# Performance work log

Measured on AMD Instinct MI355X. Metric: run time of the kernel, lower is better.

Reference implementation:

```python
import jax, jax.numpy as jnp
import numpy as np

B, SQ, SK, D, DV = 8, 2048, 4096, 512, 256

def setup_inputs() -> dict:
    key = jax.random.key(0)
    k1, k2, k3, k4, k5 = jax.random.split(key, 5)
    X = jax.random.normal(k1, (B, SQ, D), dtype=jnp.float32)
    Y = jax.random.normal(k2, (SK, D), dtype=jnp.float32)
    Z = jax.random.normal(k3, (SK, D), dtype=jnp.float32)
    # Linear weights (torch stores [out, in]); scaled like default init
    W_k = jax.random.normal(k4, (D, D), dtype=jnp.float32) / np.sqrt(D)
    W_v = jax.random.normal(k5, (DV, D), dtype=jnp.float32) / np.sqrt(D)
    return {"X": X, "Y": Y, "Z": Z, "W_k": W_k, "W_v": W_v, "rate": 0}


def reference(X, Y, Z, W_k, W_v, rate):
    # key = W_k(Y).unsqueeze(0): [1, SK, D]; value = W_v(Z).unsqueeze(0): [1, SK, DV]
    key = (Y @ W_k.T)[None]
    value = (Z @ W_v.T)[None]
    # scores = X @ key^T / sqrt(d): [B, SQ, SK] (key batch dim broadcasts)
    scale = 1.0 / jnp.sqrt(jnp.asarray(X.shape[-1], dtype=X.dtype))
    scores = jnp.matmul(X, jnp.swapaxes(key, 1, 2)) * scale
    attn = jax.nn.softmax(scores, axis=-1)
    # dropout layers act as identity in eval mode
    out = jnp.matmul(attn, value)  # [B, SQ, DV]
    return out
```

## Files before the change

kernel.cpp:

```cpp
#include <hip/hip_runtime.h>
#include <hip/hip_bf16.h>

#define NB    8
#define SQN   2048
#define SKN   4096
#define DDIM  512
#define DVDIM 256
#define NROWS (NB*SQN)
#define NS    2
#define NJ    ((SKN/64)/NS)

typedef __attribute__((ext_vector_type(8)))  short bf16x8;
typedef __attribute__((ext_vector_type(4)))  short bf16x4;
typedef __attribute__((ext_vector_type(4)))  float f32x4;
typedef __attribute__((ext_vector_type(16))) float f32x16;

__device__ __forceinline__ short f2bf(float f) {
    unsigned u = __float_as_uint(f);
    return (short)((u + 0x7FFFu + ((u >> 16) & 1u)) >> 16);
}

__device__ __forceinline__ void gload_lds16(const void* g, void* l) {
    __builtin_amdgcn_global_load_lds(
        (const __attribute__((address_space(1))) unsigned int*)g,
        (__attribute__((address_space(3))) unsigned int*)l, 16, 0, 0);
}

#define BAR_VM(N_) do {                                                       \
    asm volatile("s_waitcnt vmcnt(" #N_ ")" ::: "memory");                    \
    __builtin_amdgcn_sched_barrier(0);                                        \
    __builtin_amdgcn_s_barrier();                                             \
    __builtin_amdgcn_sched_barrier(0);                                        \
} while (0)

#define BAR_LGKM() do {                                                       \
    asm volatile("s_waitcnt lgkmcnt(0)" ::: "memory");                        \
    __builtin_amdgcn_sched_barrier(0);                                        \
    __builtin_amdgcn_s_barrier();                                             \
    __builtin_amdgcn_sched_barrier(0);                                        \
} while (0)

__global__ __launch_bounds__(256, 2) void proj_gemms(
    const float* __restrict__ Y, const float* __restrict__ Z,
    const float* __restrict__ Wk, const float* __restrict__ Wv,
    unsigned short* __restrict__ keyb, unsigned short* __restrict__ vtb)
{
    __shared__ short sA[64*128];
    __shared__ short sB[64*128];
    const float *A, *Bm;
    unsigned short* C;
    int N, m0, n0;
    if (blockIdx.z == 0) {
        A = Y; Bm = Wk; C = keyb; N = DDIM;
        m0 = blockIdx.x * 64; n0 = blockIdx.y * 64;
    } else {
        int lin = blockIdx.x * 8 + blockIdx.y;
        if (lin >= 256) return;
        A = Wv; Bm = Z; C = vtb; N = SKN;
        m0 = (lin >> 6) * 64; n0 = (lin & 63) * 64;
    }
    const int tid  = threadIdx.x;
    const int wave = tid >> 6;
    const int lane = tid & 63;
    const int quad = lane >> 4;
    const int l15  = lane & 15;

    f32x4 acc[4];
    #pragma unroll
    for (int n = 0; n < 4; ++n) { acc[n][0]=0.f; acc[n][1]=0.f; acc[n][2]=0.f; acc[n][3]=0.f; }

    float4 ra[8], rb[8];
    #pragma unroll
    for (int it = 0; it < 8; ++it) {
        int f = it*1024 + tid*4, row = f >> 7, col = f & 127;
        ra[it] = *(const float4*)(A  + (size_t)(m0+row)*DDIM + col);
        rb[it] = *(const float4*)(Bm + (size_t)(n0+row)*DDIM + col);
    }

    for (int kc = 0; kc < DDIM; kc += 128) {
        __syncthreads();
        #pragma unroll
        for (int it = 0; it < 8; ++it) {
            int f = it*1024 + tid*4;
            bf16x4 a4; a4[0]=f2bf(ra[it].x); a4[1]=f2bf(ra[it].y); a4[2]=f2bf(ra[it].z); a4[3]=f2bf(ra[it].w);
            *(bf16x4*)(sA + f) = a4;
            bf16x4 b4; b4[0]=f2bf(rb[it].x); b4[1]=f2bf(rb[it].y); b4[2]=f2bf(rb[it].z); b4[3]=f2bf(rb[it].w);
            *(bf16x4*)(sB + f) = b4;
        }
        __syncthreads();
        if (kc + 128 < DDIM) {
            #pragma unroll
            for (int it = 0; it < 8; ++it) {
                int f = it*1024 + tid*4, row = f >> 7, col = f & 127;
                ra[it] = *(const float4*)(A  + (size_t)(m0+row)*DDIM + kc + 128 + col);
                rb[it] = *(const float4*)(Bm + (size_t)(n0+row)*DDIM + kc + 128 + col);
            }
        }
        #pragma unroll
        for (int t = 0; t < 4; ++t) {
            bf16x8 af = *(const bf16x8*)(sA + (wave*16 + l15)*128 + t*32 + quad*8);
            #pragma unroll
            for (int n = 0; n < 4; ++n) {
                bf16x8 bfr = *(const bf16x8*)(sB + (n*16 + l15)*128 + t*32 + quad*8);
                acc[n] = __builtin_amdgcn_mfma_f32_16x16x32_bf16(af, bfr, acc[n], 0, 0, 0);
            }
        }
    }
    #pragma unroll
    for (int n = 0; n < 4; ++n)
        #pragma unroll
        for (int r = 0; r < 4; ++r) {
            int m  = m0 + wave*16 + quad*4 + r;
            int nn = n0 + n*16 + l15;
            C[(size_t)m*N + nn] = (unsigned short)f2bf(acc[n][r]);
        }
}

__global__ __launch_bounds__(512, 2) void attn_fused(
    const float* __restrict__ X,
    const unsigned short* __restrict__ Kb,
    const unsigned short* __restrict__ Vt,
    float* __restrict__ Opart,
    float* __restrict__ Mpart,
    float* __restrict__ Lpart)
{
    __shared__ __align__(16) char smem[100352];
    char* sV   = smem + 49152;
    char* sPex = smem + 81920;
    float* sSt = (float*)(smem + 98304);

    const int tid  = threadIdx.x;
    const int wave = tid >> 6;
    const int lane = tid & 63;
    const int l31  = lane & 31;
    const int hi   = lane >> 5;
    const int wm   = wave >> 1;
    const int wk   = wave & 1;

    const int bid   = blockIdx.x;
    const int xcd   = bid & 7;
    const int slot  = bid >> 3;
    const int split = xcd >> 2;
    const int q0    = ((xcd & 3)*32 + slot) * 128;
    const float scale = 0.04419417382415922f;

    bf16x8 qf[32];
    {
        const float* xrow = X + (size_t)(q0 + wm*32 + l31)*DDIM + hi*8;
        #pragma unroll
        for (int t = 0; t < 32; ++t) {
            float4 a = *(const float4*)(xrow + t*16);
            float4 b = *(const float4*)(xrow + t*16 + 4);
            bf16x8 q;
            q[0]=f2bf(a.x*scale); q[1]=f2bf(a.y*scale); q[2]=f2bf(a.z*scale); q[3]=f2bf(a.w*scale);
            q[4]=f2bf(b.x*scale); q[5]=f2bf(b.y*scale); q[6]=f2bf(b.z*scale); q[7]=f2bf(b.w*scale);
            qf[t] = q;
        }
    }

    f32x16 o[4];
    #pragma unroll
    for (int n = 0; n < 4; ++n)
        #pragma unroll
        for (int r = 0; r < 16; ++r) o[n][r] = 0.f;
    float m_r = -1e30f, l_r = 0.f;

    const int jt0 = split * (NJ*64);

    #define STAGE_K(jtb_, cc_, bufp_)                                         \
        do {                                                                  \
            _Pragma("unroll")                                                 \
            for (int it_ = 0; it_ < 2; ++it_) {                               \
                const char* src_ = (const char*)Kb                            \
                    + (size_t)((jtb_) + it_*32 + l31)*1024                    \
                    + (cc_)*256 + wave*32 + hi*16;                            \
                gload_lds16(src_, (bufp_) + (wave*2 + it_)*1024);             \
            }                                                                 \
        } while (0)

    #define STAGE_V(jtb_)                                                     \
        do {                                                                  \
            _Pragma("unroll")                                                 \
            for (int it_ = 0; it_ < 4; ++it_) {                               \
                const char* src_ = (const char*)Vt                            \
                    + (size_t)(wave*32 + l31)*8192                            \
                    + (size_t)((jtb_) + it_*16 + hi*8)*2;                     \
                gload_lds16(src_, sV + (wave*4 + it_)*1024);                  \
            }                                                                 \
        } while (0)

    char* q0p = smem;
    char* q1p = smem + 16384;
    char* q2p = smem + 32768;

    STAGE_K(jt0, 0, q0p);
    STAGE_K(jt0, 1, q1p);

    for (int j = 0; j < NJ; ++j) {
        const int jtb = jt0 + j*64;
        f32x16 s;
        #pragma unroll
        for (int r = 0; r < 16; ++r) s[r] = 0.f;

        #pragma unroll
        for (int c = 0; c < 4; ++c) {
            if (c == 0)      BAR_VM(2);
            else if (c == 1) BAR_VM(6);
            else if (c == 2) BAR_VM(6);
            else { if (j + 1 < NJ) BAR_VM(2); else BAR_VM(0); }

            if (c == 0)      { STAGE_K(jtb, 2, q2p); STAGE_V(jtb); }
            else if (c == 1) STAGE_K(jtb, 3, q0p);
            else if (c == 2) { if (j + 1 < NJ) STAGE_K(jtb + 64, 0, q1p); }
            else             { if (j + 1 < NJ) STAGE_K(jtb + 64, 1, q2p); }

            const char* rbuf = (c == 0) ? q0p : (c == 1) ? q1p
                             : (c == 2) ? q2p : q0p;
            const char* kb = rbuf + wk*1024 + lane*16;
            __builtin_amdgcn_s_setprio(1);
            #pragma unroll
            for (int t = 0; t < 8; ++t) {
                bf16x8 kf = *(const bf16x8*)(kb + t*2048);
                s = __builtin_amdgcn_mfma_f32_32x32x16_bf16(kf, qf[c*8+t], s, 0, 0, 0);
            }
            __builtin_amdgcn_s_setprio(0);
        }

        float tmax = fmaxf(fmaxf(fmaxf(s[0],s[1]),fmaxf(s[2],s[3])),
                           fmaxf(fmaxf(s[4],s[5]),fmaxf(s[6],s[7])));
        tmax = fmaxf(tmax, fmaxf(fmaxf(fmaxf(s[8],s[9]),fmaxf(s[10],s[11])),
                                 fmaxf(fmaxf(s[12],s[13]),fmaxf(s[14],s[15]))));
        tmax = fmaxf(tmax, __shfl_xor(tmax, 32));
        if (lane < 32) sSt[(wave*2 + 0)*32 + lane] = tmax;
        BAR_LGKM();
        float tmax_o = sSt[((wave^1)*2 + 0)*32 + l31];
        const float mn = fmaxf(m_r, fmaxf(tmax, tmax_o));
        const float alpha = __expf(m_r - mn);
        float tsum = 0.f;
        #pragma unroll
        for (int r = 0; r < 16; ++r) { float pv = __expf(s[r] - mn); s[r] = pv; tsum += pv; }
        tsum += __shfl_xor(tsum, 32);

        bf16x8 pf[2];
        #pragma unroll
        for (int ks = 0; ks < 2; ++ks) {
            int wA, wB, wC, wD;
            asm("v_cvt_pk_bf16_f32 %0, %1, %2" : "=v"(wA) : "v"(s[8*ks+0]), "v"(s[8*ks+1]));
            asm("v_cvt_pk_bf16_f32 %0, %1, %2" : "=v"(wB) : "v"(s[8*ks+2]), "v"(s[8*ks+3]));
            asm("v_cvt_pk_bf16_f32 %0, %1, %2" : "=v"(wC) : "v"(s[8*ks+4]), "v"(s[8*ks+5]));
            asm("v_cvt_pk_bf16_f32 %0, %1, %2" : "=v"(wD) : "v"(s[8*ks+6]), "v"(s[8*ks+7]));
            asm("v_permlane32_swap_b32 %0, %1" : "+v"(wA), "+v"(wC));
            asm("v_permlane32_swap_b32 %0, %1" : "+v"(wB), "+v"(wD));
            union { int w[4]; bf16x8 v; } u;
            u.w[0] = wA; u.w[1] = wB; u.w[2] = wC; u.w[3] = wD;
            pf[ks] = u.v;
        }
        *(bf16x8*)(sPex + (wm*4 + wk*2 + 0)*1024 + lane*16) = pf[0];
        *(bf16x8*)(sPex + (wm*4 + wk*2 + 1)*1024 + lane*16) = pf[1];
        if (lane < 32) sSt[(wave*2 + 1)*32 + lane] = tsum;
        BAR_LGKM();
        float tsum_o = sSt[((wave^1)*2 + 1)*32 + l31];
        l_r = l_r*alpha + (tsum + tsum_o);
        m_r = mn;
        if (__any(alpha < 1.f)) {
            #pragma unroll
            for (int r = 0; r < 16; ++r) {
                int row = (r&3) + 8*(r>>2) + 4*hi;
                float ar = __shfl(alpha, row);
                #pragma unroll
                for (int n = 0; n < 4; ++n) o[n][r] *= ar;
            }
        }

        const char* vb = sV + wk*16384 + lane*16;
        const char* pb = sPex + wm*4096 + lane*16;
        __builtin_amdgcn_s_setprio(1);
        #pragma unroll
        for (int g = 0; g < 4; ++g) {
            bf16x8 pa = ((g >> 1) == wk) ? pf[g & 1]
                        : *(const bf16x8*)(pb + g*1024);
            #pragma unroll
            for (int n = 0; n < 4; ++n) {
                bf16x8 vf = *(const bf16x8*)(vb + (n*4 + g)*1024);
                o[n] = __builtin_amdgcn_mfma_f32_32x32x16_bf16(pa, vf, o[n], 0, 0, 0);
            }
        }
        __builtin_amdgcn_s_setprio(0);

        char* tp = q0p; q0p = q1p; q1p = q2p; q2p = tp;
    }
    #undef STAGE_K
    #undef STAGE_V

    const size_t base = (size_t)split * NROWS;
    const int gr0 = q0 + wm*32;
    if (wk == 0 && lane < 32) {
        Mpart[base + gr0 + lane] = m_r;
        Lpart[base + gr0 + lane] = l_r;
    }
    #pragma unroll
    for (int r = 0; r < 16; ++r) {
        int row = (r&3) + 8*(r>>2) + 4*hi;
        float* orow = Opart + (base + gr0 + row) * (size_t)DVDIM + wk*128;
        #pragma unroll
        for (int n = 0; n < 4; ++n)
            orow[n*32 + l31] = o[n][r];
    }
}

__global__ void combine_splits(
    const float* __restrict__ Opart, const float* __restrict__ Mpart,
    const float* __restrict__ Lpart, float* __restrict__ out)
{
    const int row = blockIdx.x * 4 + (threadIdx.x >> 6);
    const int dv4 = (threadIdx.x & 63) * 4;
    float M = -1e30f;
    #pragma unroll
    for (int s = 0; s < NS; ++s) M = fmaxf(M, Mpart[(size_t)s*NROWS + row]);
    float denom = 0.f;
    float4 acc = make_float4(0.f, 0.f, 0.f, 0.f);
    #pragma unroll
    for (int s = 0; s < NS; ++s) {
        float w = __expf(Mpart[(size_t)s*NROWS + row] - M);
        denom += Lpart[(size_t)s*NROWS + row] * w;
        float4 ov = *(const float4*)(Opart + ((size_t)s*NROWS + row)*DVDIM + dv4);
        acc.x += ov.x*w; acc.y += ov.y*w; acc.z += ov.z*w; acc.w += ov.w*w;
    }
    float inv = 1.0f / denom;
    *(float4*)(out + (size_t)row*DVDIM + dv4)
        = make_float4(acc.x*inv, acc.y*inv, acc.z*inv, acc.w*inv);
}

extern "C" void kernel_launch(void* const* d_in, const int* in_sizes, int n_in,
                              void* d_out, int out_size, void* d_ws, size_t ws_size,
                              hipStream_t stream) {
    const float* X  = (const float*)d_in[0];
    const float* Y  = (const float*)d_in[1];
    const float* Z  = (const float*)d_in[2];
    const float* Wk = (const float*)d_in[3];
    const float* Wv = (const float*)d_in[4];
    float* out = (float*)d_out;

    char* ws = (char*)d_ws;
    unsigned short* keyb = (unsigned short*)ws;
    unsigned short* vtb  = (unsigned short*)(ws + (4u<<20));
    float* Opart = (float*)(ws + (6u<<20));
    float* Mpart = (float*)(ws + (6u<<20) + (size_t)NS*NROWS*DVDIM*4);
    float* Lpart = Mpart + (size_t)NS*NROWS;

    proj_gemms<<<dim3(64, 8, 2), dim3(256), 0, stream>>>(Y, Z, Wk, Wv, keyb, vtb);
    attn_fused<<<dim3(256), dim3(512), 0, stream>>>(
        X, keyb, vtb, Opart, Mpart, Lpart);
    combine_splits<<<dim3(NROWS/4), dim3(256), 0, stream>>>(Opart, Mpart, Lpart, out);
}
```

Measured before the change: 266.8 us.

## Halve attention block to 64 query rows with double-buffered K staging

Shrinks each attention workgroup from 8 waves/128 query rows to 4 waves/64 rows and doubles the grid, so each wave stages twice as many K/V chunks. The K pipeline goes from a three-buffer rotation with partial waits to two alternating buffers with mostly full vmcnt waits, reducing LDS per block. The aim is more blocks per CU and finer scheduling, at the cost of loading each K/V tile twice as often overall and having less load/compute overlap.

```diff
diff --git a/kernel.cpp b/kernel.cpp
--- a/kernel.cpp
+++ b/kernel.cpp
@@ -116,7 +116,7 @@
         }
 }
 
-__global__ __launch_bounds__(512, 2) void attn_fused(
+__global__ __launch_bounds__(256, 2) void attn_fused(
     const float* __restrict__ X,
     const unsigned short* __restrict__ Kb,
     const unsigned short* __restrict__ Vt,
@@ -124,10 +124,12 @@
     float* __restrict__ Mpart,
     float* __restrict__ Lpart)
 {
-    __shared__ __align__(16) char smem[100352];
-    char* sV   = smem + 49152;
-    char* sPex = smem + 81920;
-    float* sSt = (float*)(smem + 98304);
+    __shared__ __align__(16) char smem[74752];
+    char* b0   = smem;
+    char* b1   = smem + 16384;
+    char* sV   = smem + 32768;
+    char* sPex = smem + 65536;
+    float* sSt = (float*)(smem + 73728);
 
     const int tid  = threadIdx.x;
     const int wave = tid >> 6;
@@ -141,7 +143,7 @@
     const int xcd   = bid & 7;
     const int slot  = bid >> 3;
     const int split = xcd >> 2;
-    const int q0    = ((xcd & 3)*32 + slot) * 128;
+    const int q0    = ((xcd & 3)*64 + slot) * 64;
     const float scale = 0.04419417382415922f;
 
     bf16x8 qf[32];
@@ -170,31 +172,39 @@
     #define STAGE_K(jtb_, cc_, bufp_)                                         \
         do {                                                                  \
             _Pragma("unroll")                                                 \
-            for (int it_ = 0; it_ < 2; ++it_) {                               \
+            for (int it_ = 0; it_ < 4; ++it_) {                               \
                 const char* src_ = (const char*)Kb                            \
-                    + (size_t)((jtb_) + it_*32 + l31)*1024                    \
-                    + (cc_)*256 + wave*32 + hi*16;                            \
-                gload_lds16(src_, (bufp_) + (wave*2 + it_)*1024);             \
+                    + (size_t)((jtb_) + (it_&1)*32 + l31)*1024                \
+                    + (cc_)*256 + wave*64 + (it_>>1)*32 + hi*16;              \
+                gload_lds16(src_, (bufp_) + (wave*4 + it_)*1024);             \
             }                                                                 \
         } while (0)
 
     #define STAGE_V(jtb_)                                                     \
         do {                                                                  \
             _Pragma("unroll")                                                 \
-            for (int it_ = 0; it_ < 4; ++it_) {                               \
+            for (int it_ = 0; it_ < 8; ++it_) {                               \
                 const char* src_ = (const char*)Vt                            \
-                    + (size_t)(wave*32 + l31)*8192                            \
-                    + (size_t)((jtb_) + it_*16 + hi*8)*2;                     \
-                gload_lds16(src_, sV + (wave*4 + it_)*1024);                  \
+                    + (size_t)((wave*2 + (it_>>2))*32 + l31)*8192             \
+                    + (size_t)((jtb_) + (it_&3)*16 + hi*8)*2;                 \
+                gload_lds16(src_, sV + (wave*8 + it_)*1024);                  \
             }                                                                 \
         } while (0)
 
-    char* q0p = smem;
-    char* q1p = smem + 16384;
-    char* q2p = smem + 32768;
-
-    STAGE_K(jt0, 0, q0p);
-    STAGE_K(jt0, 1, q1p);
+    #define QK8(cc_, bufp_)                                                   \
+        do {                                                                  \
+            const char* kb_ = (bufp_) + wk*1024 + lane*16;                    \
+            __builtin_amdgcn_s_setprio(1);                                    \
+            _Pragma("unroll")                                                 \
+            for (int t_ = 0; t_ < 8; ++t_) {                                  \
+                bf16x8 kf_ = *(const bf16x8*)(kb_ + t_*2048);                 \
+                s = __builtin_amdgcn_mfma_f32_32x32x16_bf16(                  \
+                        kf_, qf[(cc_)*8 + t_], s, 0, 0, 0);                   \
+            }                                                                 \
+            __builtin_amdgcn_s_setprio(0);                                    \
+        } while (0)
+
+    STAGE_K(jt0, 0, b0);
 
     for (int j = 0; j < NJ; ++j) {
         const int jtb = jt0 + j*64;
@@ -202,29 +212,19 @@
         #pragma unroll
         for (int r = 0; r < 16; ++r) s[r] = 0.f;
 
-        #pragma unroll
-        for (int c = 0; c < 4; ++c) {
-            if (c == 0)      BAR_VM(2);
-            else if (c == 1) BAR_VM(6);
-            else if (c == 2) BAR_VM(6);
-            else { if (j + 1 < NJ) BAR_VM(2); else BAR_VM(0); }
-
-            if (c == 0)      { STAGE_K(jtb, 2, q2p); STAGE_V(jtb); }
-            else if (c == 1) STAGE_K(jtb, 3, q0p);
-            else if (c == 2) { if (j + 1 < NJ) STAGE_K(jtb + 64, 0, q1p); }
-            else             { if (j + 1 < NJ) STAGE_K(jtb + 64, 1, q2p); }
-
-            const char* rbuf = (c == 0) ? q0p : (c == 1) ? q1p
-                             : (c == 2) ? q2p : q0p;
-            const char* kb = rbuf + wk*1024 + lane*16;
-            __builtin_amdgcn_s_setprio(1);
-            #pragma unroll
-            for (int t = 0; t < 8; ++t) {
-                bf16x8 kf = *(const bf16x8*)(kb + t*2048);
-                s = __builtin_amdgcn_mfma_f32_32x32x16_bf16(kf, qf[c*8+t], s, 0, 0, 0);
-            }
-            __builtin_amdgcn_s_setprio(0);
-        }
+        BAR_VM(0);
+        STAGE_K(jtb, 1, b1);
+        STAGE_V(jtb);
+        QK8(0, b0);
+        BAR_VM(8);
+        STAGE_K(jtb, 2, b0);
+        QK8(1, b1);
+        BAR_VM(0);
+        STAGE_K(jtb, 3, b1);
+        QK8(2, b0);
+        BAR_VM(0);
+        if (j + 1 < NJ) STAGE_K(jtb + 64, 0, b0);
+        QK8(3, b1);
 
         float tmax = fmaxf(fmaxf(fmaxf(s[0],s[1]),fmaxf(s[2],s[3])),
                            fmaxf(fmaxf(s[4],s[5]),fmaxf(s[6],s[7])));
@@ -286,11 +286,10 @@
             }
         }
         __builtin_amdgcn_s_setprio(0);
-
-        char* tp = q0p; q0p = q1p; q1p = q2p; q2p = tp;
     }
     #undef STAGE_K
     #undef STAGE_V
+    #undef QK8
 
     const size_t base = (size_t)split * NROWS;
     const int gr0 = q0 + wm*32;
@@ -349,7 +348,7 @@
     float* Lpart = Mpart + (size_t)NS*NROWS;
 
     proj_gemms<<<dim3(64, 8, 2), dim3(256), 0, stream>>>(Y, Z, Wk, Wv, keyb, vtb);
-    attn_fused<<<dim3(256), dim3(512), 0, stream>>>(
+    attn_fused<<<dim3(512), dim3(256), 0, stream>>>(
         X, keyb, vtb, Opart, Mpart, Lpart);
     combine_splits<<<dim3(NROWS/4), dim3(256), 0, stream>>>(Opart, Mpart, Lpart, out);
 }
```

Result: slower. 354.2 us (+32.7%).

## Load K and V fragments directly to registers instead of LDS staging

Applied to the files above, without the earlier changes.

Replaces the triple-buffered global-to-LDS staging of K and V, with its per-chunk barriers, by direct per-wave global loads into double-buffered register fragments. A quarter of Q moves to a per-wave LDS region to free registers for these fragments. The softmax moves to exp2 with log2e folded into the Q scale, and the running max is only rescaled when a tile max exceeds it by more than 8. The cost is that each wave now reads K and V from global or L2 memory itself rather than sharing them through LDS, so global traffic goes up and load latency is exposed in the MFMA loops.

```diff
diff --git a/kernel.cpp b/kernel.cpp
--- a/kernel.cpp
+++ b/kernel.cpp
@@ -19,19 +19,6 @@
     unsigned u = __float_as_uint(f);
     return (short)((u + 0x7FFFu + ((u >> 16) & 1u)) >> 16);
 }
-
-__device__ __forceinline__ void gload_lds16(const void* g, void* l) {
-    __builtin_amdgcn_global_load_lds(
-        (const __attribute__((address_space(1))) unsigned int*)g,
-        (__attribute__((address_space(3))) unsigned int*)l, 16, 0, 0);
-}
-
-#define BAR_VM(N_) do {                                                       \
-    asm volatile("s_waitcnt vmcnt(" #N_ ")" ::: "memory");                    \
-    __builtin_amdgcn_sched_barrier(0);                                        \
-    __builtin_amdgcn_s_barrier();                                             \
-    __builtin_amdgcn_sched_barrier(0);                                        \
-} while (0)
 
 #define BAR_LGKM() do {                                                       \
     asm volatile("s_waitcnt lgkmcnt(0)" ::: "memory");                        \
@@ -124,10 +111,10 @@
     float* __restrict__ Mpart,
     float* __restrict__ Lpart)
 {
-    __shared__ __align__(16) char smem[100352];
-    char* sV   = smem + 49152;
-    char* sPex = smem + 81920;
-    float* sSt = (float*)(smem + 98304);
+    __shared__ __align__(16) char smem[83968];
+    char* sQw  = smem + (threadIdx.x >> 6)*8192;
+    char* sPex = smem + 65536;
+    float* sSt = (float*)(smem + 81920);
 
     const int tid  = threadIdx.x;
     const int wave = tid >> 6;
@@ -142,9 +129,9 @@
     const int slot  = bid >> 3;
     const int split = xcd >> 2;
     const int q0    = ((xcd & 3)*32 + slot) * 128;
-    const float scale = 0.04419417382415922f;
-
-    bf16x8 qf[32];
+    const float scale = 0.04419417382415922f * 1.4426950408889634f;
+
+    bf16x8 qf[24];
     {
         const float* xrow = X + (size_t)(q0 + wm*32 + l31)*DDIM + hi*8;
         #pragma unroll
@@ -154,7 +141,8 @@
             bf16x8 q;
             q[0]=f2bf(a.x*scale); q[1]=f2bf(a.y*scale); q[2]=f2bf(a.z*scale); q[3]=f2bf(a.w*scale);
             q[4]=f2bf(b.x*scale); q[5]=f2bf(b.y*scale); q[6]=f2bf(b.z*scale); q[7]=f2bf(b.w*scale);
-            qf[t] = q;
+            if (t < 24) qf[t] = q;
+            else        *(bf16x8*)(sQw + (t - 24)*1024 + lane*16) = q;
         }
     }
 
@@ -167,34 +155,14 @@
 
     const int jt0 = split * (NJ*64);
 
-    #define STAGE_K(jtb_, cc_, bufp_)                                         \
-        do {                                                                  \
-            _Pragma("unroll")                                                 \
-            for (int it_ = 0; it_ < 2; ++it_) {                               \
-                const char* src_ = (const char*)Kb                            \
-                    + (size_t)((jtb_) + it_*32 + l31)*1024                    \
-                    + (cc_)*256 + wave*32 + hi*16;                            \
-                gload_lds16(src_, (bufp_) + (wave*2 + it_)*1024);             \
-            }                                                                 \
-        } while (0)
-
-    #define STAGE_V(jtb_)                                                     \
-        do {                                                                  \
-            _Pragma("unroll")                                                 \
-            for (int it_ = 0; it_ < 4; ++it_) {                               \
-                const char* src_ = (const char*)Vt                            \
-                    + (size_t)(wave*32 + l31)*8192                            \
-                    + (size_t)((jtb_) + it_*16 + hi*8)*2;                     \
-                gload_lds16(src_, sV + (wave*4 + it_)*1024);                  \
-            }                                                                 \
-        } while (0)
-
-    char* q0p = smem;
-    char* q1p = smem + 16384;
-    char* q2p = smem + 32768;
-
-    STAGE_K(jt0, 0, q0p);
-    STAGE_K(jt0, 1, q1p);
+    const unsigned short* krow = Kb + (size_t)(jt0 + wk*32 + l31)*DDIM + hi*8;
+    const unsigned short* vrow = Vt + (size_t)(wk*128 + l31)*SKN + hi*8;
+
+    bf16x8 kf[2][4];
+    bf16x8 vf[2][4];
+
+    #pragma unroll
+    for (int t = 0; t < 4; ++t) kf[0][t] = *(const bf16x8*)(krow + t*16);
 
     for (int j = 0; j < NJ; ++j) {
         const int jtb = jt0 + j*64;
@@ -203,28 +171,27 @@
         for (int r = 0; r < 16; ++r) s[r] = 0.f;
 
         #pragma unroll
-        for (int c = 0; c < 4; ++c) {
-            if (c == 0)      BAR_VM(2);
-            else if (c == 1) BAR_VM(6);
-            else if (c == 2) BAR_VM(6);
-            else { if (j + 1 < NJ) BAR_VM(2); else BAR_VM(0); }
-
-            if (c == 0)      { STAGE_K(jtb, 2, q2p); STAGE_V(jtb); }
-            else if (c == 1) STAGE_K(jtb, 3, q0p);
-            else if (c == 2) { if (j + 1 < NJ) STAGE_K(jtb + 64, 0, q1p); }
-            else             { if (j + 1 < NJ) STAGE_K(jtb + 64, 1, q2p); }
-
-            const char* rbuf = (c == 0) ? q0p : (c == 1) ? q1p
-                             : (c == 2) ? q2p : q0p;
-            const char* kb = rbuf + wk*1024 + lane*16;
+        for (int h = 0; h < 8; ++h) {
+            if (h < 7) {
+                const unsigned short* ka = krow + (h + 1)*64;
+                #pragma unroll
+                for (int t = 0; t < 4; ++t)
+                    kf[(h + 1) & 1][t] = *(const bf16x8*)(ka + t*16);
+            }
             __builtin_amdgcn_s_setprio(1);
             #pragma unroll
-            for (int t = 0; t < 8; ++t) {
-                bf16x8 kf = *(const bf16x8*)(kb + t*2048);
-                s = __builtin_amdgcn_mfma_f32_32x32x16_bf16(kf, qf[c*8+t], s, 0, 0, 0);
+            for (int t = 0; t < 4; ++t) {
+                bf16x8 qv = (h < 6) ? qf[h*4 + t]
+                    : *(const bf16x8*)(sQw + ((h - 6)*4 + t)*1024 + lane*16);
+                s = __builtin_amdgcn_mfma_f32_32x32x16_bf16(
+                        kf[h & 1][t], qv, s, 0, 0, 0);
             }
             __builtin_amdgcn_s_setprio(0);
         }
+
+        #pragma unroll
+        for (int n = 0; n < 4; ++n)
+            vf[0][n] = *(const bf16x8*)(vrow + (size_t)(n*32)*SKN + jtb);
 
         float tmax = fmaxf(fmaxf(fmaxf(s[0],s[1]),fmaxf(s[2],s[3])),
                            fmaxf(fmaxf(s[4],s[5]),fmaxf(s[6],s[7])));
@@ -234,11 +201,12 @@
         if (lane < 32) sSt[(wave*2 + 0)*32 + lane] = tmax;
         BAR_LGKM();
         float tmax_o = sSt[((wave^1)*2 + 0)*32 + l31];
-        const float mn = fmaxf(m_r, fmaxf(tmax, tmax_o));
-        const float alpha = __expf(m_r - mn);
+        const float tj   = fmaxf(tmax, tmax_o);
+        const bool  upd  = tj > m_r + 8.0f;
+        const float mn   = upd ? tj : m_r;
         float tsum = 0.f;
         #pragma unroll
-        for (int r = 0; r < 16; ++r) { float pv = __expf(s[r] - mn); s[r] = pv; tsum += pv; }
+        for (int r = 0; r < 16; ++r) { float pv = exp2f(s[r] - mn); s[r] = pv; tsum += pv; }
         tsum += __shfl_xor(tsum, 32);
 
         bf16x8 pf[2];
@@ -258,11 +226,18 @@
         *(bf16x8*)(sPex + (wm*4 + wk*2 + 0)*1024 + lane*16) = pf[0];
         *(bf16x8*)(sPex + (wm*4 + wk*2 + 1)*1024 + lane*16) = pf[1];
         if (lane < 32) sSt[(wave*2 + 1)*32 + lane] = tsum;
+
+        if (j + 1 < NJ) {
+            krow += 64*DDIM;
+            #pragma unroll
+            for (int t = 0; t < 4; ++t) kf[0][t] = *(const bf16x8*)(krow + t*16);
+        }
         BAR_LGKM();
         float tsum_o = sSt[((wave^1)*2 + 1)*32 + l31];
+        float alpha  = upd ? exp2f(m_r - mn) : 1.0f;
         l_r = l_r*alpha + (tsum + tsum_o);
         m_r = mn;
-        if (__any(alpha < 1.f)) {
+        if (__any(upd)) {
             #pragma unroll
             for (int r = 0; r < 16; ++r) {
                 int row = (r&3) + 8*(r>>2) + 4*hi;
@@ -272,25 +247,25 @@
             }
         }
 
-        const char* vb = sV + wk*16384 + lane*16;
         const char* pb = sPex + wm*4096 + lane*16;
-        __builtin_amdgcn_s_setprio(1);
         #pragma unroll
         for (int g = 0; g < 4; ++g) {
+            if (g < 3) {
+                #pragma unroll
+                for (int n = 0; n < 4; ++n)
+                    vf[(g + 1) & 1][n] = *(const bf16x8*)(vrow
+                        + (size_t)(n*32)*SKN + jtb + (g + 1)*16);
+            }
             bf16x8 pa = ((g >> 1) == wk) ? pf[g & 1]
                         : *(const bf16x8*)(pb + g*1024);
-            #pragma unroll
-            for (int n = 0; n < 4; ++n) {
-                bf16x8 vf = *(const bf16x8*)(vb + (n*4 + g)*1024);
-                o[n] = __builtin_amdgcn_mfma_f32_32x32x16_bf16(pa, vf, o[n], 0, 0, 0);
-            }
-        }
-        __builtin_amdgcn_s_setprio(0);
-
-        char* tp = q0p; q0p = q1p; q1p = q2p; q2p = tp;
-    }
-    #undef STAGE_K
-    #undef STAGE_V
+            __builtin_amdgcn_s_setprio(1);
+            #pragma unroll
+            for (int n = 0; n < 4; ++n)
+                o[n] = __builtin_amdgcn_mfma_f32_32x32x16_bf16(
+                        pa, vf[g & 1][n], o[n], 0, 0, 0);
+            __builtin_amdgcn_s_setprio(0);
+        }
+    }
 
     const size_t base = (size_t)split * NROWS;
     const int gr0 = q0 + wm*32;
@@ -321,7 +296,7 @@
     float4 acc = make_float4(0.f, 0.f, 0.f, 0.f);
     #pragma unroll
     for (int s = 0; s < NS; ++s) {
-        float w = __expf(Mpart[(size_t)s*NROWS + row] - M);
+        float w = exp2f(Mpart[(size_t)s*NROWS + row] - M);
         denom += Lpart[(size_t)s*NROWS + row] * w;
         float4 ov = *(const float4*)(Opart + ((size_t)s*NROWS + row)*DVDIM + dv4);
         acc.x += ov.x*w; acc.y += ov.y*w; acc.z += ov.z*w; acc.w += ov.w*w;
```

Measured after the change: 478.0 us. 79.2% more time.
